# Optimization experiments

Hardware: AMD Instinct MI355X
Metric: run time of the kernel (lower is better)

The kernel has to match this reference:

```python
import jax, jax.numpy as jnp
import numpy as np

B, S, HID = 2, 2048, 1024
H, D = 16, HID // 16  # heads, head_dim
ROPE_BASE = 10000.0


def setup_inputs() -> dict:
    key = jax.random.key(0)
    k1, k2, k3, k4 = jax.random.split(key, 4)
    scale = 1.0 / np.sqrt(HID)
    return {
        "hidden_states": jax.random.normal(k1, (B, S, HID), dtype=jnp.float32),
        "attention_mask": jnp.zeros((B, 1, 1, S), dtype=jnp.float32),
        "Wq": jax.random.normal(k2, (HID, HID), dtype=jnp.float32) * scale,
        "Wk": jax.random.normal(k3, (HID, HID), dtype=jnp.float32) * scale,
        "Wv": jax.random.normal(k4, (HID, HID), dtype=jnp.float32) * scale,
    }


def _rope_cos_sin(seq_len, dim, dtype):
    inv_freq = 1.0 / (ROPE_BASE ** (jnp.arange(0, dim, 2, dtype=jnp.float32) / dim))
    freqs = jnp.arange(seq_len, dtype=jnp.float32)[:, None] * inv_freq[None, :]  # (S, D/2)
    emb = jnp.concatenate([freqs, freqs], axis=-1)  # (S, D)
    return jnp.cos(emb).astype(dtype), jnp.sin(emb).astype(dtype)


def _rotate_half(x):
    x1, x2 = jnp.split(x, 2, axis=-1)
    return jnp.concatenate([-x2, x1], axis=-1)


def reference(hidden_states, attention_mask, Wq, Wk, Wv):
    b, s, _ = hidden_states.shape
    # QKV projections (no bias), split into heads: (b, H, s, D)
    def proj(W):
        return jnp.einsum('bse,de->bsd', hidden_states, W).reshape(b, s, H, D).transpose(0, 2, 1, 3)
    q, k, v = proj(Wq), proj(Wk), proj(Wv)
    # Rotary embedding on q, k over sequence positions
    cos, sin = _rope_cos_sin(s, D, hidden_states.dtype)  # (s, D)
    cos = cos[None, None]  # (1,1,s,D)
    sin = sin[None, None]
    q = q * cos + _rotate_half(q) * sin
    k = k * cos + _rotate_half(k) * sin
    # Scaled dot-product attention with additive mask
    scores = jnp.einsum('bhqd,bhkd->bhqk', q, k) / jnp.sqrt(jnp.asarray(D, hidden_states.dtype))
    scores = scores + attention_mask
    probs = jax.nn.softmax(scores, axis=-1)  # dropout p=0 (eval) -> identity
    ctx = jnp.einsum('bhqk,bhkd->bhqd', probs, v)
    return ctx.transpose(0, 2, 1, 3).reshape(b, s, H * D)
```

## Files before the change

kernel.cpp:

```cpp
#include <hip/hip_runtime.h>
#include <stdint.h>

typedef unsigned short u16;
typedef short bf16x8 __attribute__((ext_vector_type(8)));
typedef float f32x4 __attribute__((ext_vector_type(4)));
typedef float f32x16 __attribute__((ext_vector_type(16)));

#define S_ 2048
#define HID_ 1024
#define H_ 16
#define D_ 64

#define LOG2E 1.4426950408889634f
#define SCALE_LOG2 0.18033688011112042f
#define MAXC_LOG2 11.541560327111707f

__device__ __forceinline__ u16 f2bf(float f) {
  uint32_t x = __builtin_bit_cast(uint32_t, f);
  uint32_t r = (x + 0x7fffu + ((x >> 16) & 1u)) >> 16;
  return (u16)r;
}
__device__ __forceinline__ uint32_t packbf2(float a, float b) {
  return (uint32_t)f2bf(a) | ((uint32_t)f2bf(b) << 16);
}
__device__ __forceinline__ uint32_t permpack(float a, float b) {
  return __builtin_amdgcn_perm(__builtin_bit_cast(uint32_t, b),
                               __builtin_bit_cast(uint32_t, a), 0x07060302u);
}

__device__ __forceinline__ void gl2lds16(const void* g, void* l) {
  __builtin_amdgcn_global_load_lds(
      (const __attribute__((address_space(1))) unsigned int*)g,
      (__attribute__((address_space(3))) unsigned int*)l, 16, 0, 0);
}

#define NX_ (1 << 20)
#define NW_ (1 << 18)
#define NROPE_ 65536
__global__ void prep_kernel(const float* __restrict__ X, const float* __restrict__ Wq,
                            const float* __restrict__ Wk, const float* __restrict__ Wv,
                            const float* __restrict__ mask, u16* __restrict__ Xb,
                            u16* __restrict__ Wqb, u16* __restrict__ Wkb,
                            u16* __restrict__ Wvb, float* __restrict__ cos_t,
                            float* __restrict__ sin_t, float* __restrict__ mask2) {
  int i = blockIdx.x * 256 + threadIdx.x;
  if (i < NX_ + 3 * NW_) {
    const float* src;
    u16* dst;
    int off;
    if (i < NX_) {
      src = X; dst = Xb; off = i;
    } else if (i < NX_ + NW_) {
      src = Wq; dst = Wqb; off = i - NX_;
    } else if (i < NX_ + 2 * NW_) {
      src = Wk; dst = Wkb; off = i - NX_ - NW_;
    } else {
      src = Wv; dst = Wvb; off = i - NX_ - 2 * NW_;
    }
    float4 v = ((const float4*)src)[off];
    uint2 packed;
    packed.x = packbf2(v.x, v.y);
    packed.y = packbf2(v.z, v.w);
    ((uint2*)dst)[off] = packed;
  } else if (i < NX_ + 3 * NW_ + NROPE_) {
    int t = i - (NX_ + 3 * NW_);
    int s = t >> 5, j = t & 31;
    float invf = powf(10000.0f, -(float)j * (1.0f / 32.0f));
    float ang = (float)s * invf;
    cos_t[t] = cosf(ang);
    sin_t[t] = sinf(ang);
  } else {
    int t = i - (NX_ + 3 * NW_ + NROPE_);
    mask2[t] = fmaf(mask[t], LOG2E, -MAXC_LOG2);
  }
}

__global__ __launch_bounds__(256) void qkv_gemm_kernel(
    const u16* __restrict__ X, const u16* __restrict__ Wq, const u16* __restrict__ Wk,
    const u16* __restrict__ Wv, const float* __restrict__ cos_t,
    const float* __restrict__ sin_t, u16* __restrict__ Q, u16* __restrict__ K,
    u16* __restrict__ Vt) {
  __shared__ char smem[65536];
  int tid = threadIdx.x;
  int lane = tid & 63, wave = tid >> 6;
  int wm = wave >> 1, wn = wave & 1;
  int quad = lane >> 4, l16 = lane & 15;
  int which = blockIdx.x >> 3;
  int nbase = (blockIdx.x & 7) * 128;
  int mbase = blockIdx.y * 128;
  const u16* W = (which == 0) ? Wq : (which == 1) ? Wk : Wv;

#pragma unroll
  for (int it = 0; it < 4; ++it) {
    int i = it * 256 + tid;
    int r = i >> 3, gs = i & 7, gsrc = gs ^ (r & 7);
    gl2lds16(X + (size_t)(mbase + r) * HID_ + gsrc * 8, smem + i * 16);
    gl2lds16(W + (size_t)(nbase + r) * HID_ + gsrc * 8, smem + 32768 + i * 16);
  }

  f32x4 acc[4][4] = {};

  for (int kk = 0; kk < 16; ++kk) {
    char* As = smem + (kk & 1) * 16384;
    char* Bs = smem + 32768 + (kk & 1) * 16384;
    __syncthreads();

    if (kk < 15) {
      int k0n = (kk + 1) * 64;
      char* An = smem + ((kk + 1) & 1) * 16384;
      char* Bn = smem + 32768 + ((kk + 1) & 1) * 16384;
#pragma unroll
      for (int it = 0; it < 4; ++it) {
        int i = it * 256 + tid;
        int r = i >> 3, gs = i & 7, gsrc = gs ^ (r & 7);
        gl2lds16(X + (size_t)(mbase + r) * HID_ + k0n + gsrc * 8, An + i * 16);
        gl2lds16(W + (size_t)(nbase + r) * HID_ + k0n + gsrc * 8, Bn + i * 16);
      }
    }

#pragma unroll
    for (int kh = 0; kh < 2; ++kh) {
      bf16x8 afrag[4], bfrag[4];
#pragma unroll
      for (int i4 = 0; i4 < 4; ++i4) {
        int r = wm * 64 + i4 * 16 + l16;
        int L = r * 8 + ((kh * 4 + quad) ^ (r & 7));
        afrag[i4] = *(const bf16x8*)(As + L * 16);
      }
#pragma unroll
      for (int j4 = 0; j4 < 4; ++j4) {
        int r = wn * 64 + j4 * 16 + l16;
        int L = r * 8 + ((kh * 4 + quad) ^ (r & 7));
        bfrag[j4] = *(const bf16x8*)(Bs + L * 16);
      }
      if (which == 2) {
#pragma unroll
        for (int i4 = 0; i4 < 4; ++i4)
#pragma unroll
          for (int j4 = 0; j4 < 4; ++j4)
            acc[i4][j4] = __builtin_amdgcn_mfma_f32_16x16x32_bf16(afrag[i4], bfrag[j4],
                                                                  acc[i4][j4], 0, 0, 0);
      } else {
#pragma unroll
        for (int i4 = 0; i4 < 4; ++i4)
#pragma unroll
          for (int j4 = 0; j4 < 4; ++j4)
            acc[i4][j4] = __builtin_amdgcn_mfma_f32_16x16x32_bf16(bfrag[j4], afrag[i4],
                                                                  acc[i4][j4], 0, 0, 0);
      }
    }
  }

  if (which == 2) {
#pragma unroll
    for (int i4 = 0; i4 < 4; ++i4)
#pragma unroll
      for (int j4 = 0; j4 < 4; ++j4) {
        int m = mbase + wm * 64 + i4 * 16 + quad * 4;
        int n = nbase + wn * 64 + j4 * 16 + l16;
        int b = m >> 11, s0 = m & 2047;
        int h = n >> 6, d = n & 63;
        uint2 pk;
        pk.x = packbf2(acc[i4][j4][0], acc[i4][j4][1]);
        pk.y = packbf2(acc[i4][j4][2], acc[i4][j4][3]);
        *(uint2*)(Vt + (((size_t)(b * H_ + h)) * D_ + d) * S_ + s0) = pk;
      }
  } else {
    u16* dst = (which == 0) ? Q : K;
#pragma unroll
    for (int i4 = 0; i4 < 4; ++i4)
#pragma unroll
      for (int j4 = 0; j4 < 2; ++j4) {
        int m = mbase + wm * 64 + i4 * 16 + l16;
        int n1 = nbase + wn * 64 + j4 * 16 + quad * 4;
        int b = m >> 11, s = m & 2047;
        int h = n1 >> 6, d1 = n1 & 63;
        float4 c4 = *(const float4*)(cos_t + s * 32 + d1);
        float4 s4 = *(const float4*)(sin_t + s * 32 + d1);
        float y1[4], y2[4];
#pragma unroll
        for (int r = 0; r < 4; ++r) {
          float cr = ((const float*)&c4)[r], sr = ((const float*)&s4)[r];
          float x1 = acc[i4][j4][r], x2 = acc[i4][j4 + 2][r];
          y1[r] = x1 * cr - x2 * sr;
          y2[r] = x2 * cr + x1 * sr;
        }
        size_t base = ((size_t)(b * H_ + h) * S_ + s) * D_;
        uint2 p1, p2;
        p1.x = packbf2(y1[0], y1[1]);
        p1.y = packbf2(y1[2], y1[3]);
        p2.x = packbf2(y2[0], y2[1]);
        p2.y = packbf2(y2[2], y2[3]);
        *(uint2*)(dst + base + d1) = p1;
        *(uint2*)(dst + base + d1 + 32) = p2;
      }
  }
}

__device__ __forceinline__ void pv32(const char* Pw, const char* Vp, int q31, int hf,
                                     const bf16x8& ones, f32x16& o0, f32x16& o1,
                                     f32x16& lacc) {
  int l7 = q31 & 7;
  bf16x8 pf[4];
#pragma unroll
  for (int c = 0; c < 4; ++c) {
    int ch = (2 * c + hf) ^ l7;
    pf[c] = *(const bf16x8*)(Pw + q31 * 128 + ch * 16);
  }
#pragma unroll
  for (int c = 0; c < 4; ++c)
    lacc = __builtin_amdgcn_mfma_f32_32x32x16_bf16(pf[c], ones, lacc, 0, 0, 0);
#pragma unroll
  for (int c = 0; c < 4; ++c) {
    int ch = (2 * c + hf) ^ l7;
    bf16x8 v0 = *(const bf16x8*)(Vp + q31 * 128 + ch * 16);
    bf16x8 v1 = *(const bf16x8*)(Vp + (32 + q31) * 128 + ch * 16);
    o0 = __builtin_amdgcn_mfma_f32_32x32x16_bf16(pf[c], v0, o0, 0, 0, 0);
    o1 = __builtin_amdgcn_mfma_f32_32x32x16_bf16(pf[c], v1, o1, 0, 0, 0);
  }
}

__global__ __launch_bounds__(256, 2) void flash_kernel(
    const u16* __restrict__ Q, const u16* __restrict__ K, const u16* __restrict__ Vt,
    const float* __restrict__ mask2, float* __restrict__ out) {
  __shared__ char smem[65536];
  int tid = threadIdx.x, wave = tid >> 6;
  int lane = tid & 63;
  int q31 = lane & 31, hf = lane >> 5, l7 = lane & 7;
  int bh = blockIdx.y, b = bh >> 4, hh = bh & 15;
  int qw = blockIdx.x * 128 + wave * 32;
  char* Pw = smem + 49152 + wave * 4096;
  const float* m2row = mask2 + b * S_;
  const u16* Kbase = K + (size_t)bh * S_ * D_;
  const u16* Vbase = Vt + (size_t)bh * D_ * S_;

  bf16x8 qfrag[4];
  {
    const u16* qp = Q + ((size_t)bh * S_ + qw + q31) * D_ + 8 * hf;
#pragma unroll
    for (int c = 0; c < 4; ++c) qfrag[c] = *(const bf16x8*)(qp + 16 * c);
  }
  bf16x8 ones;
#pragma unroll
  for (int j = 0; j < 8; ++j) ones[j] = (short)0x3f80;

  f32x16 o0 = {}, o1 = {}, lacc = {};

#pragma unroll
  for (int it = 0; it < 2; ++it) {
    int i = it * 256 + tid;
    int r = i >> 3, gs = i & 7, gsrc = gs ^ (r & 7);
    gl2lds16(Kbase + (size_t)r * D_ + gsrc * 8, smem + i * 16);
    gl2lds16(Vbase + (size_t)r * S_ + gsrc * 8, smem + 8192 + i * 16);
  }
  float4 mvt[8];
#pragma unroll
  for (int kb = 0; kb < 2; ++kb)
#pragma unroll
    for (int g = 0; g < 4; ++g)
      mvt[kb * 4 + g] = *(const float4*)(m2row + kb * 32 + g * 8 + hf * 4);

  for (int kt = 0; kt < 32; ++kt) {
    char* Ks = smem + (kt % 3) * 16384;
    __syncthreads();

    if (kt < 31) {
      char* Kn = smem + ((kt + 1) % 3) * 16384;
      char* Vn = Kn + 8192;
      int nb = (kt + 1) * 64;
#pragma unroll
      for (int it = 0; it < 2; ++it) {
        int i = it * 256 + tid;
        int r = i >> 3, gs = i & 7, gsrc = gs ^ (r & 7);
        gl2lds16(Kbase + (size_t)(nb + r) * D_ + gsrc * 8, Kn + i * 16);
        gl2lds16(Vbase + (size_t)r * S_ + nb + gsrc * 8, Vn + i * 16);
      }
    }

    if (kt > 0) pv32(Pw, smem + ((kt + 2) % 3) * 16384 + 8192, q31, hf, ones, o0, o1, lacc);

    f32x16 s0 = {}, s1 = {};
#pragma unroll
    for (int c = 0; c < 4; ++c) {
      int ch = (2 * c + hf) ^ l7;
      bf16x8 k0 = *(const bf16x8*)(Ks + q31 * 128 + ch * 16);
      bf16x8 k1 = *(const bf16x8*)(Ks + (32 + q31) * 128 + ch * 16);
      s0 = __builtin_amdgcn_mfma_f32_32x32x16_bf16(k0, qfrag[c], s0, 0, 0, 0);
      s1 = __builtin_amdgcn_mfma_f32_32x32x16_bf16(k1, qfrag[c], s1, 0, 0, 0);
    }

#pragma unroll
    for (int kb = 0; kb < 2; ++kb) {
#pragma unroll
      for (int g = 0; g < 4; ++g) {
        float pf4[4];
#pragma unroll
        for (int r0 = 0; r0 < 4; ++r0) {
          float sv = kb ? s1[g * 4 + r0] : s0[g * 4 + r0];
          pf4[r0] = __builtin_amdgcn_exp2f(
              fmaf(sv, SCALE_LOG2, ((const float*)&mvt[kb * 4 + g])[r0]));
        }
        uint2 pk;
        pk.x = permpack(pf4[0], pf4[1]);
        pk.y = permpack(pf4[2], pf4[3]);
        int chunk8 = (8 * kb + 2 * g + hf) ^ (2 * l7);
        *(uint2*)(Pw + q31 * 128 + chunk8 * 8) = pk;
      }
    }

    if (kt < 31) {
#pragma unroll
      for (int kb = 0; kb < 2; ++kb)
#pragma unroll
        for (int g = 0; g < 4; ++g)
          mvt[kb * 4 + g] =
              *(const float4*)(m2row + (kt + 1) * 64 + kb * 32 + g * 8 + hf * 4);
    }
  }

  pv32(Pw, smem + 16384 + 8192, q31, hf, ones, o0, o1, lacc);

#pragma unroll
  for (int g = 0; g < 4; ++g)
#pragma unroll
    for (int r0 = 0; r0 < 4; ++r0) {
      int reg = g * 4 + r0;
      int q = qw + r0 + 8 * g + 4 * hf;
      float invl = 1.0f / lacc[reg];
      size_t base = (((size_t)b * S_ + q) * H_ + hh) * D_;
      out[base + q31] = o0[reg] * invl;
      out[base + 32 + q31] = o1[reg] * invl;
    }
}

extern "C" void kernel_launch(void* const* d_in, const int* in_sizes, int n_in,
                              void* d_out, int out_size, void* d_ws, size_t ws_size,
                              hipStream_t stream) {
  const float* hid = (const float*)d_in[0];
  const float* mask = (const float*)d_in[1];
  const float* Wq = (const float*)d_in[2];
  const float* Wk = (const float*)d_in[3];
  const float* Wv = (const float*)d_in[4];
  float* out = (float*)d_out;
  char* ws = (char*)d_ws;

  u16* Xbf = (u16*)ws;
  u16* Wqb = (u16*)(ws + (8u << 20));
  u16* Wkb = (u16*)(ws + (10u << 20));
  u16* Wvb = (u16*)(ws + (12u << 20));
  u16* Qb = (u16*)(ws + (14u << 20));
  u16* Kb = (u16*)(ws + (22u << 20));
  u16* Vtb = (u16*)(ws + (30u << 20));
  float* cos_t = (float*)(ws + (38u << 20));
  float* sin_t = (float*)(ws + (38u << 20) + (256u << 10));
  float* mask2 = (float*)(ws + (38u << 20) + (512u << 10));

  prep_kernel<<<7440, 256, 0, stream>>>(hid, Wq, Wk, Wv, mask, Xbf, Wqb, Wkb, Wvb,
                                        cos_t, sin_t, mask2);
  qkv_gemm_kernel<<<dim3(24, 32), 256, 0, stream>>>(Xbf, Wqb, Wkb, Wvb, cos_t, sin_t,
                                                    Qb, Kb, Vtb);
  flash_kernel<<<dim3(16, 32), 256, 0, stream>>>(Qb, Kb, Vtb, mask2, out);
}
```

Baseline: 172.6 us.

## Keep softmax P in registers via lane shuffles, transpose PV MFMA, stage output

The attention kernel no longer writes the exponentiated scores P to shared memory and reads them back a tile later. It packs P into bf16 registers and exchanges halves between lane groups with shuffles, then feeds them directly as the B operand of transposed PV and row-sum MFMAs in the same iteration. This drops the per-wave P buffer and the one-tile software pipeline, cutting shared memory from 64KB to 34KB and the K/V ring from triple to double buffering. The epilogue stages the normalized output through shared memory so each lane writes contiguous float4 rows instead of strided scalars. The trade-off is less overlap between PV and the next QK, plus extra shuffle instructions.

```diff
diff --git a/kernel.cpp b/kernel.cpp
--- a/kernel.cpp
+++ b/kernel.cpp
@@ -197,46 +197,21 @@
   }
 }
 
-__device__ __forceinline__ void pv32(const char* Pw, const char* Vp, int q31, int hf,
-                                     const bf16x8& ones, f32x16& o0, f32x16& o1,
-                                     f32x16& lacc) {
-  int l7 = q31 & 7;
-  bf16x8 pf[4];
-#pragma unroll
-  for (int c = 0; c < 4; ++c) {
-    int ch = (2 * c + hf) ^ l7;
-    pf[c] = *(const bf16x8*)(Pw + q31 * 128 + ch * 16);
-  }
-#pragma unroll
-  for (int c = 0; c < 4; ++c)
-    lacc = __builtin_amdgcn_mfma_f32_32x32x16_bf16(pf[c], ones, lacc, 0, 0, 0);
-#pragma unroll
-  for (int c = 0; c < 4; ++c) {
-    int ch = (2 * c + hf) ^ l7;
-    bf16x8 v0 = *(const bf16x8*)(Vp + q31 * 128 + ch * 16);
-    bf16x8 v1 = *(const bf16x8*)(Vp + (32 + q31) * 128 + ch * 16);
-    o0 = __builtin_amdgcn_mfma_f32_32x32x16_bf16(pf[c], v0, o0, 0, 0, 0);
-    o1 = __builtin_amdgcn_mfma_f32_32x32x16_bf16(pf[c], v1, o1, 0, 0, 0);
-  }
-}
-
 __global__ __launch_bounds__(256, 2) void flash_kernel(
     const u16* __restrict__ Q, const u16* __restrict__ K, const u16* __restrict__ Vt,
     const float* __restrict__ mask2, float* __restrict__ out) {
-  __shared__ char smem[65536];
-  int tid = threadIdx.x, wave = tid >> 6;
-  int lane = tid & 63;
-  int q31 = lane & 31, hf = lane >> 5, l7 = lane & 7;
+  __shared__ char smem[34816];
+  int tid = threadIdx.x, wave = tid >> 6, lane = tid & 63;
+  int lq = lane & 31, hf = lane >> 5, l7 = lane & 7;
   int bh = blockIdx.y, b = bh >> 4, hh = bh & 15;
   int qw = blockIdx.x * 128 + wave * 32;
-  char* Pw = smem + 49152 + wave * 4096;
   const float* m2row = mask2 + b * S_;
   const u16* Kbase = K + (size_t)bh * S_ * D_;
   const u16* Vbase = Vt + (size_t)bh * D_ * S_;
 
   bf16x8 qfrag[4];
   {
-    const u16* qp = Q + ((size_t)bh * S_ + qw + q31) * D_ + 8 * hf;
+    const u16* qp = Q + ((size_t)bh * S_ + qw + lq) * D_ + 8 * hf;
 #pragma unroll
     for (int c = 0; c < 4; ++c) qfrag[c] = *(const bf16x8*)(qp + 16 * c);
   }
@@ -261,11 +236,12 @@
       mvt[kb * 4 + g] = *(const float4*)(m2row + kb * 32 + g * 8 + hf * 4);
 
   for (int kt = 0; kt < 32; ++kt) {
-    char* Ks = smem + (kt % 3) * 16384;
+    char* Ks = smem + (kt & 1) * 16384;
+    char* Vs = Ks + 8192;
     __syncthreads();
 
     if (kt < 31) {
-      char* Kn = smem + ((kt + 1) % 3) * 16384;
+      char* Kn = smem + ((kt + 1) & 1) * 16384;
       char* Vn = Kn + 8192;
       int nb = (kt + 1) * 64;
 #pragma unroll
@@ -277,34 +253,52 @@
       }
     }
 
-    if (kt > 0) pv32(Pw, smem + ((kt + 2) % 3) * 16384 + 8192, q31, hf, ones, o0, o1, lacc);
-
     f32x16 s0 = {}, s1 = {};
 #pragma unroll
     for (int c = 0; c < 4; ++c) {
       int ch = (2 * c + hf) ^ l7;
-      bf16x8 k0 = *(const bf16x8*)(Ks + q31 * 128 + ch * 16);
-      bf16x8 k1 = *(const bf16x8*)(Ks + (32 + q31) * 128 + ch * 16);
+      bf16x8 k0 = *(const bf16x8*)(Ks + lq * 128 + ch * 16);
+      bf16x8 k1 = *(const bf16x8*)(Ks + (32 + lq) * 128 + ch * 16);
       s0 = __builtin_amdgcn_mfma_f32_32x32x16_bf16(k0, qfrag[c], s0, 0, 0, 0);
       s1 = __builtin_amdgcn_mfma_f32_32x32x16_bf16(k1, qfrag[c], s1, 0, 0, 0);
     }
 
-#pragma unroll
-    for (int kb = 0; kb < 2; ++kb) {
-#pragma unroll
-      for (int g = 0; g < 4; ++g) {
-        float pf4[4];
-#pragma unroll
-        for (int r0 = 0; r0 < 4; ++r0) {
-          float sv = kb ? s1[g * 4 + r0] : s0[g * 4 + r0];
-          pf4[r0] = __builtin_amdgcn_exp2f(
-              fmaf(sv, SCALE_LOG2, ((const float*)&mvt[kb * 4 + g])[r0]));
-        }
-        uint2 pk;
-        pk.x = permpack(pf4[0], pf4[1]);
-        pk.y = permpack(pf4[2], pf4[3]);
-        int chunk8 = (8 * kb + 2 * g + hf) ^ (2 * l7);
-        *(uint2*)(Pw + q31 * 128 + chunk8 * 8) = pk;
+    uint32_t pk[2][8];
+#pragma unroll
+    for (int t = 0; t < 2; ++t) {
+#pragma unroll
+      for (int m = 0; m < 8; ++m) {
+        const float* mv4 = (const float*)&mvt[t * 4 + (m >> 1)];
+        float sa = t ? s1[2 * m] : s0[2 * m];
+        float sb = t ? s1[2 * m + 1] : s0[2 * m + 1];
+        float e0 = __builtin_amdgcn_exp2f(fmaf(sa, SCALE_LOG2, mv4[2 * (m & 1)]));
+        float e1 = __builtin_amdgcn_exp2f(fmaf(sb, SCALE_LOG2, mv4[2 * (m & 1) + 1]));
+        pk[t][m] = permpack(e0, e1);
+      }
+    }
+
+#pragma unroll
+    for (int t = 0; t < 2; ++t) {
+#pragma unroll
+      for (int u = 0; u < 2; ++u) {
+        int c = 2 * t + u;
+        uint32_t send0 = hf ? pk[t][4 * u] : pk[t][4 * u + 2];
+        uint32_t send1 = hf ? pk[t][4 * u + 1] : pk[t][4 * u + 3];
+        uint32_t recv0 = (uint32_t)__shfl_xor((int)send0, 32);
+        uint32_t recv1 = (uint32_t)__shfl_xor((int)send1, 32);
+        union { uint32_t w[4]; bf16x8 v; } pf;
+        pf.w[0] = hf ? recv0 : pk[t][4 * u];
+        pf.w[1] = hf ? recv1 : pk[t][4 * u + 1];
+        pf.w[2] = hf ? pk[t][4 * u + 2] : recv0;
+        pf.w[3] = hf ? pk[t][4 * u + 3] : recv1;
+
+        lacc = __builtin_amdgcn_mfma_f32_32x32x16_bf16(ones, pf.v, lacc, 0, 0, 0);
+
+        int chv = (2 * c + hf) ^ l7;
+        bf16x8 v0 = *(const bf16x8*)(Vs + lq * 128 + chv * 16);
+        bf16x8 v1 = *(const bf16x8*)(Vs + (32 + lq) * 128 + chv * 16);
+        o0 = __builtin_amdgcn_mfma_f32_32x32x16_bf16(v0, pf.v, o0, 0, 0, 0);
+        o1 = __builtin_amdgcn_mfma_f32_32x32x16_bf16(v1, pf.v, o1, 0, 0, 0);
       }
     }
 
@@ -318,19 +312,29 @@
     }
   }
 
-  pv32(Pw, smem + 16384 + 8192, q31, hf, ones, o0, o1, lacc);
-
+  __syncthreads();
+  float invl = 1.0f / lacc[0];
+  float* T = (float*)(smem + wave * 8704);
 #pragma unroll
   for (int g = 0; g < 4; ++g)
 #pragma unroll
-    for (int r0 = 0; r0 < 4; ++r0) {
-      int reg = g * 4 + r0;
-      int q = qw + r0 + 8 * g + 4 * hf;
-      float invl = 1.0f / lacc[reg];
-      size_t base = (((size_t)b * S_ + q) * H_ + hh) * D_;
-      out[base + q31] = o0[reg] * invl;
-      out[base + 32 + q31] = o1[reg] * invl;
-    }
+    for (int r0 = 0; r0 < 4; r0 += 2) {
+      int reg = 4 * g + r0;
+      int d0 = r0 + 8 * g + 4 * hf;
+      float2 w0, w1;
+      w0.x = o0[reg] * invl;
+      w0.y = o0[reg + 1] * invl;
+      w1.x = o1[reg] * invl;
+      w1.y = o1[reg + 1] * invl;
+      *(float2*)(T + lq * 68 + d0) = w0;
+      *(float2*)(T + lq * 68 + 32 + d0) = w1;
+    }
+  int qr = lane >> 1, half = lane & 1;
+  const float* Tr = (const float*)(smem + wave * 8704) + qr * 68 + half * 32;
+  float* gout = out + (((size_t)b * S_ + qw + qr) * H_ + hh) * D_ + half * 32;
+#pragma unroll
+  for (int i = 0; i < 8; ++i)
+    *(float4*)(gout + 4 * i) = *(const float4*)(Tr + 4 * i);
 }
 
 extern "C" void kernel_launch(void* const* d_in, const int* in_sizes, int n_in,
```

After: 179.2 us. 3.8% more time.
